# Optimization experiments

Measured on AMD Instinct MI355X. Metric: run time of the kernel, lower is better.

## Reference

```python
import jax, jax.numpy as jnp
import numpy as np

N = 64      # SSM state size (hidden_size)
H = 1024    # channels
L = 2048    # sequence length
BATCH = 8


def setup_inputs() -> dict:
    key = jax.random.key(0)
    ks = jax.random.split(key, 12)
    s = 1.0 / np.sqrt(N)
    n = jnp.arange(N, dtype=jnp.float32)
    return {
        "r": jax.random.normal(ks[0], (BATCH, L, H), dtype=jnp.float32),
        "B_re": jax.random.normal(ks[1], (N,), dtype=jnp.float32) * s,
        "B_im": jax.random.normal(ks[2], (N,), dtype=jnp.float32) * s,
        "C_re": jax.random.normal(ks[3], (H, N), dtype=jnp.float32) * s,
        "C_im": jax.random.normal(ks[4], (H, N), dtype=jnp.float32) * s,
        "P_re": jax.random.normal(ks[5], (N,), dtype=jnp.float32) * s,
        "P_im": jax.random.normal(ks[6], (N,), dtype=jnp.float32) * s,
        "Q_re": jax.random.normal(ks[7], (N,), dtype=jnp.float32) * s,
        "Q_im": jax.random.normal(ks[8], (N,), dtype=jnp.float32) * s,
        # HiPPO-LegS-like diagonal: negative real part for stability, imag ~ pi*n
        "diag_re": -0.5 * jnp.ones((N,), dtype=jnp.float32),
        "diag_im": jnp.pi * (n - N / 2.0),
        "step": jnp.array([1e-3], dtype=jnp.float32),
        "D": jnp.zeros((1,), dtype=jnp.float32),
    }


def _dplr_kernel(Bc, Cc, Pc, Qc, Lam, step, seq_len):
    # Standard S4 DPLR generating function evaluated at roots of unity,
    # then inverse FFT -> real convolution kernel K_c of shape (H, L).
    z = jnp.exp(-2j * jnp.pi * jnp.arange(seq_len) / seq_len).astype(jnp.complex64)  # (L,)
    g = (2.0 / step) * (1.0 - z) / (1.0 + z)                                          # (L,)
    cden = 1.0 / (g[:, None] - Lam[None, :])                                          # (L,N) Cauchy denom
    k00 = jnp.einsum('hn,ln->hl', Cc * Bc, cden)   # (H,L)
    k01 = jnp.einsum('hn,ln->hl', Cc * Pc, cden)   # (H,L)
    k10 = jnp.einsum('n,ln->l', Qc * Bc, cden)     # (L,)
    k11 = jnp.einsum('n,ln->l', Qc * Pc, cden)     # (L,)
    at_roots = (2.0 / (1.0 + z)) * (k00 - k01 * (k10 / (1.0 + k11)))  # (H,L)
    return jnp.fft.ifft(at_roots, axis=-1).real


def reference(r, B_re, B_im, C_re, C_im, P_re, P_im, Q_re, Q_im,
              diag_re, diag_im, step, D):
    step_c = jnp.maximum(step[0], 1e-6)
    Bc = B_re + 1j * B_im
    Cc = C_re + 1j * C_im
    Pc = P_re + 1j * P_im
    Qc = Q_re + 1j * Q_im
    Lam = diag_re + 1j * diag_im
    seq_len = r.shape[1]
    K = _dplr_kernel(Bc, Cc, Pc, Qc, Lam, step_c, seq_len)  # (H, L)
    # causal FFT convolution along the sequence axis
    nfft = 2 * seq_len
    Kf = jnp.fft.rfft(K, n=nfft, axis=-1)            # (H, nfft//2+1)
    uf = jnp.fft.rfft(r, n=nfft, axis=1)             # (B, nfft//2+1, H)
    h1 = jnp.fft.irfft(uf * Kf.T[None], n=nfft, axis=1)[:, :seq_len]  # (B,L,H)
    y1 = h1 + D[0] * r
    return jax.nn.gelu(y1, approximate=False)
```

## Files before the change

kernel.cpp:

```cpp
#include <hip/hip_runtime.h>
#include <math.h>

#define SSM_N 64
#define SSM_H 1024
#define SSM_L 2048
#define SSM_B 8
#define FFTN 2048
#define NT 256
#define KFS 2052

#define PSWZ(a) ((a) ^ (((a) >> 4) & 15))

typedef float f2 __attribute__((ext_vector_type(2)));
static __device__ __forceinline__ f2 mkf2(float a, float b){ f2 v; v.x = a; v.y = b; return v; }

static __device__ __forceinline__ f2 cmul(f2 a, f2 b){
  return mkf2(-a.y, a.y) * mkf2(b.y, b.x) + mkf2(a.x, a.x) * b;
}
static __device__ __forceinline__ f2 cconj(f2 a){ return mkf2(a.x, -a.y); }

template<bool INV> static __device__ __forceinline__ f2 mul_mi(f2 a){
  return INV ? mkf2(-a.y, a.x) : mkf2(a.y, -a.x);
}
template<bool INV> static __device__ __forceinline__ f2 mul_w81(f2 a){
  const float r = 0.70710678118654752440f;
  return INV ? (r * mkf2(a.x - a.y, a.y + a.x)) : (r * mkf2(a.x + a.y, a.y - a.x));
}
template<bool INV> static __device__ __forceinline__ f2 mul_w83(f2 a){
  const float r = 0.70710678118654752440f;
  return INV ? (r * mkf2(-(a.x + a.y), a.x - a.y)) : (r * mkf2(a.y - a.x, -(a.x + a.y)));
}

#define W8C0 1.f
#define W8S0 0.f
#define W8C1 0.92387953251f
#define W8S1 (-0.38268343236f)
#define W8C2 0.70710678119f
#define W8S2 (-0.70710678119f)
#define W8C3 0.38268343236f
#define W8S3 (-0.92387953251f)
#define W8C4 0.f
#define W8S4 (-1.f)
#define W8C5 (-0.38268343236f)
#define W8S5 (-0.92387953251f)
#define W8C6 (-0.70710678119f)
#define W8S6 (-0.70710678119f)
#define W8C7 (-0.92387953251f)
#define W8S7 (-0.38268343236f)

template<bool INV>
static __device__ __forceinline__ void bfly8_store(f2* __restrict__ dst, const f2* __restrict__ tw,
                                                   f2* x, int j, int base, int S)
{
  f2 t0=x[0]+x[4], t4=x[0]-x[4];
  f2 t1=x[1]+x[5], t5=x[1]-x[5];
  f2 t2=x[2]+x[6], t6=x[2]-x[6];
  f2 t3=x[3]+x[7], t7=x[3]-x[7];
  f2 b0=t0+t2, b2=t0-t2, b1=t1+t3, b3=t1-t3;
  f2 mb3 = mul_mi<INV>(b3);
  f2 y0=b0+b1, y4=b0-b1, y2=b2+mb3, y6=b2-mb3;
  f2 v1 = mul_w81<INV>(t5), v2 = mul_mi<INV>(t6), v3 = mul_w83<INV>(t7);
  f2 a0=t4+v2, a2=t4-v2, a1=v1+v3, a3=v1-v3;
  f2 ma3 = mul_mi<INV>(a3);
  f2 y1=a0+a1, y5=a0-a1, y3=a2+ma3, y7=a2-ma3;
  f2 w1 = tw[j];
  if (INV) w1.y = -w1.y;
  f2 w2 = cmul(w1,w1);
  f2 w3 = cmul(w2,w1);
  f2 w4 = cmul(w2,w2);
  f2 w5 = cmul(w3,w2);
  f2 w6 = cmul(w3,w3);
  f2 w7 = cmul(w4,w3);
  dst[PSWZ(base)]     = y0;
  dst[PSWZ(base+S)]   = cmul(y1,w1);
  dst[PSWZ(base+2*S)] = cmul(y2,w2);
  dst[PSWZ(base+3*S)] = cmul(y3,w3);
  dst[PSWZ(base+4*S)] = cmul(y4,w4);
  dst[PSWZ(base+5*S)] = cmul(y5,w5);
  dst[PSWZ(base+6*S)] = cmul(y6,w6);
  dst[PSWZ(base+7*S)] = cmul(y7,w7);
}

template<bool INV, bool ZTOP>
static __device__ __forceinline__ void stage8_first(const f2* __restrict__ src, f2* __restrict__ dst,
                                                    const f2* __restrict__ tw, int t, int st)
{
  const f2* sp = src + st;
  f2 x[8];
  if (ZTOP) {
    #pragma unroll
    for (int q = 0; q < 4; ++q) { x[q] = sp[256*q]; x[q+4] = mkf2(0.f, 0.f); }
  } else {
    #pragma unroll
    for (int q = 0; q < 8; ++q) x[q] = sp[256*q];
  }
  bfly8_store<INV>(dst, tw, x, t, t*8, 1);
}

template<bool INV, int S>
static __device__ __forceinline__ void stage8_mid(const f2* __restrict__ src, f2* __restrict__ dst,
                                                  const f2* __restrict__ tw, int t, int st)
{
  const f2* sp = src + st;
  f2 x[8];
  #pragma unroll
  for (int q = 0; q < 8; ++q) x[q] = sp[256*q];
  int i = t & (S-1);
  int j = t - i;
  bfly8_store<INV>(dst, tw, x, j, i + j*8, S);
}

template<bool INV, bool HALFOUT>
static __device__ __forceinline__ void stage4f(const f2* __restrict__ src, f2* __restrict__ dst, int st)
{
  #pragma unroll
  for (int hh = 0; hh < 2; ++hh) {
    const f2* sp = src + st + 256*hh;
    f2* wp = dst + st + 256*hh;
    f2 x0=sp[0], x1=sp[512], x2=sp[1024], x3=sp[1536];
    f2 a0=x0+x2, a2=x0-x2, a1=x1+x3, a3=x1-x3;
    f2 m = mul_mi<INV>(a3);
    wp[0]   = a0+a1;
    wp[512] = a2+m;
    if (!HALFOUT) {
      wp[1024] = a0-a1;
      wp[1536] = a2-m;
    }
  }
}

template<bool INV, bool ZTOP, bool HALFOUT>
static __device__ void fft2048(f2* A, f2* B, const f2* tw, int t, int st)
{
  __syncthreads();
  stage8_first<INV, ZTOP>(A, B, tw, t, st);
  __syncthreads();
  stage8_mid<INV, 8>(B, A, tw, t, st);
  __syncthreads();
  stage8_mid<INV, 64>(A, B, tw, t, st);
  __syncthreads();
  stage4f<INV, HALFOUT>(B, A, st);
  __syncthreads();
}

static __device__ __forceinline__ void init_tw(f2* tw, int t)
{
  float s, c;
  sincosf(-6.2831853071795864769f * (float)t / (float)FFTN, &s, &c);
  tw[t] = mkf2(c, s);
}

__global__ __launch_bounds__(256) void kernel_cden(
    const float* __restrict__ B_re, const float* __restrict__ B_im,
    const float* __restrict__ P_re, const float* __restrict__ P_im,
    const float* __restrict__ Q_re, const float* __restrict__ Q_im,
    const float* __restrict__ diag_re, const float* __restrict__ diag_im,
    const float* __restrict__ step,
    f2* __restrict__ cdenT, f2* __restrict__ f2v, f2* __restrict__ facv)
{
  int gid = blockIdx.x * blockDim.x + threadIdx.x;
  int l = gid >> 3, s = gid & 7;
  double stepc = (double)step[0]; if (stepc < 1e-6) stepc = 1e-6;
  double ang = -2.0 * 3.14159265358979323846 * (double)l / (double)SSM_L;
  double zr = cos(ang), zi = sin(ang);
  double dr = 1.0 + zr, di = zi;
  double nr = 1.0 - zr, ni = -zi;
  double den = dr*dr + di*di;
  double i2s = 2.0 / stepc;
  double gr = i2s * (nr*dr + ni*di) / den;
  double gi = i2s * (ni*dr - nr*di) / den;
  double k10r=0.0, k10i=0.0, k11r=0.0, k11i=0.0;
  #pragma unroll
  for (int q = 0; q < 8; ++q) {
    int n = s*8 + q;
    double ar = gr - (double)diag_re[n];
    double ai = gi - (double)diag_im[n];
    double d2 = ar*ar + ai*ai;
    double cr = ar/d2, ci = -ai/d2;
    cdenT[n*SSM_L + l] = mkf2((float)cr, (float)ci);
    double qr = (double)Q_re[n], qi = (double)Q_im[n];
    double br = (double)B_re[n], bi = (double)B_im[n];
    double pr = (double)P_re[n], pi = (double)P_im[n];
    double qbr = qr*br - qi*bi, qbi = qr*bi + qi*br;
    double qpr = qr*pr - qi*pi, qpi = qr*pi + qi*pr;
    k10r += qbr*cr - qbi*ci; k10i += qbr*ci + qbi*cr;
    k11r += qpr*cr - qpi*ci; k11i += qpr*ci + qpi*cr;
  }
  #pragma unroll
  for (int off = 1; off < 8; off <<= 1) {
    k10r += __shfl_xor(k10r, off);
    k10i += __shfl_xor(k10i, off);
    k11r += __shfl_xor(k11r, off);
    k11i += __shfl_xor(k11i, off);
  }
  if (s == 0) {
    f2v[l] = mkf2((float)(2.0*dr/den), (float)(-2.0*di/den));
    double er = 1.0 + k11r, ei = k11i;
    double ed = er*er + ei*ei;
    facv[l] = mkf2((float)((k10r*er + k10i*ei)/ed), (float)((k10i*er - k10r*ei)/ed));
  }
}

__global__ __launch_bounds__(NT, 2) void kgemm(
    const float* __restrict__ C_re, const float* __restrict__ C_im,
    const float* __restrict__ B_re, const float* __restrict__ B_im,
    const float* __restrict__ P_re, const float* __restrict__ P_im,
    const f2* __restrict__ cdenT, const f2* __restrict__ f2v, const f2* __restrict__ facv,
    f2* __restrict__ atr)
{
  __shared__ f2 cbs[256];
  int t = threadIdx.x;
  int h0 = blockIdx.x * 2;
  if (t < 128) {
    int h = h0 + (t >> 6), n = t & 63;
    f2 cc = mkf2(C_re[h*SSM_N + n], C_im[h*SSM_N + n]);
    cbs[t]       = cmul(cc, mkf2(B_re[n], B_im[n]));
    cbs[128 + t] = cmul(cc, mkf2(P_re[n], P_im[n]));
  }
  __syncthreads();
  f2 k00[2][8], k01[2][8];
  #pragma unroll
  for (int h = 0; h < 2; ++h)
    #pragma unroll
    for (int i = 0; i < 8; ++i) { k00[h][i] = mkf2(0.f,0.f); k01[h][i] = mkf2(0.f,0.f); }
  for (int n = 0; n < SSM_N; ++n) {
    f2 cd[8];
    #pragma unroll
    for (int i = 0; i < 8; ++i) cd[i] = cdenT[n*SSM_L + t + i*NT];
    #pragma unroll
    for (int h = 0; h < 2; ++h) {
      f2 cb = cbs[h*64 + n], cp = cbs[128 + h*64 + n];
      #pragma unroll
      for (int i = 0; i < 8; ++i) {
        k00[h][i] = k00[h][i] + cmul(cb, cd[i]);
        k01[h][i] = k01[h][i] + cmul(cp, cd[i]);
      }
    }
  }
  #pragma unroll
  for (int h = 0; h < 2; ++h) {
    f2* arow = atr + (size_t)(h0 + h) * SSM_L;
    #pragma unroll
    for (int i = 0; i < 8; ++i) {
      int l = t + i*NT;
      arow[l] = cmul(f2v[l], k00[h][i] - cmul(k01[h][i], facv[l]));
    }
  }
}

__global__ __launch_bounds__(NT, 4) void kfft(const f2* __restrict__ atr, f2* __restrict__ Kf)
{
  __shared__ f2 bufA[FFTN];
  __shared__ f2 bufB[FFTN];
  __shared__ f2 tw[256];
  int t = threadIdx.x;
  int st = PSWZ(t);
  int h = blockIdx.x;
  init_tw(tw, t);
  const f2* arow = atr + (size_t)h * SSM_L;
  #pragma unroll
  for (int i = 0; i < 8; ++i) {
    int n = t + i*NT;
    bufA[PSWZ(n)] = arow[n];
  }
  fft2048<true, false, false>(bufA, bufB, tw, t, st);
  float sb, cb;
  sincosf(-3.14159265358979f * (float)t / (float)FFTN, &sb, &cb);
  f2 base = mkf2(cb, sb);
  const float scale = 1.0f / (float)FFTN;
  {
    const float Wc[8] = {W8C0,W8C1,W8C2,W8C3,W8C4,W8C5,W8C6,W8C7};
    const float Ws[8] = {W8S0,W8S1,W8S2,W8S3,W8S4,W8S5,W8S6,W8S7};
    #pragma unroll
    for (int i = 0; i < 8; ++i) {
      int n = t + i*NT;
      float K = bufA[PSWZ(n)].x * scale;
      f2 c = cmul(base, mkf2(Wc[i], Ws[i]));
      bufB[PSWZ(n)] = K * c;
    }
  }
  fft2048<false, false, true>(bufB, bufA, tw, t, st);
  f2* krow = Kf + (size_t)h * KFS;
  #pragma unroll
  for (int i = 0; i < 4; ++i) {
    int m = t + i*NT;
    krow[2*m+1] = bufB[PSWZ(m)];
  }
  #pragma unroll
  for (int i = 0; i < 4; ++i) {
    int m = t + i*NT;
    if (m == 0) {
      krow[0]    = mkf2(arow[0].x, 0.f);
      krow[FFTN] = mkf2(arow[FFTN/2].x, 0.f);
    } else {
      krow[2*m] = 0.5f * (arow[m] + cconj(arow[FFTN - m]));
    }
  }
}

__global__ __launch_bounds__(256) void ktranspose(const float* __restrict__ src, float* __restrict__ dst)
{
  __shared__ float til[64][65];
  int t = threadIdx.x, tx = t & 15, ty = t >> 4;
  int h0 = blockIdx.x * 64, l0 = blockIdx.y * 64, b = blockIdx.z;
  const float4* s4 = (const float4*)(src + ((size_t)b*SSM_L + l0)*SSM_H + h0);
  #pragma unroll
  for (int i = 0; i < 4; ++i) {
    int lr = ty + 16*i;
    float4 v = s4[(size_t)lr*(SSM_H/4) + tx];
    til[lr][4*tx+0]=v.x; til[lr][4*tx+1]=v.y; til[lr][4*tx+2]=v.z; til[lr][4*tx+3]=v.w;
  }
  __syncthreads();
  float4* d4 = (float4*)(dst + ((size_t)b*SSM_H + h0)*SSM_L + l0);
  #pragma unroll
  for (int i = 0; i < 4; ++i) {
    int hr = ty + 16*i;
    float4 w;
    w.x = til[4*tx+0][hr]; w.y = til[4*tx+1][hr];
    w.z = til[4*tx+2][hr]; w.w = til[4*tx+3][hr];
    d4[(size_t)hr*(SSM_L/4) + tx] = w;
  }
}

__global__ __launch_bounds__(NT, 4) void kernel_conv(float* __restrict__ rT, const f2* __restrict__ Kf,
                                                     const float* __restrict__ Dp)
{
  __shared__ f2 bufA[FFTN];
  __shared__ f2 bufB[FFTN];
  __shared__ f2 tw[256];
  int t = threadIdx.x;
  int st = PSWZ(t);
  int row = blockIdx.x;
  int h = row & (SSM_H - 1);
  float Dv = Dp[0];
  init_tw(tw, t);
  float* rrow = rT + (size_t)row * SSM_L;
  const float4* r4 = (const float4*)rrow;
  float4 vin[2];
  #pragma unroll
  for (int i = 0; i < 2; ++i) {
    int j2 = t + i*NT;
    vin[i] = r4[j2];
    bufA[PSWZ(2*j2)]   = mkf2(vin[i].x, vin[i].y);
    bufA[PSWZ(2*j2+1)] = mkf2(vin[i].z, vin[i].w);
  }
  fft2048<false, true, false>(bufA, bufB, tw, t, st);
  const f2* krow = Kf + (size_t)h * KFS;
  float sb, cb;
  sincosf(-3.14159265358979f * (float)t / (float)FFTN, &sb, &cb);
  f2 base = mkf2(cb, sb);
  {
    const float Wc[4] = {W8C0,W8C1,W8C2,W8C3};
    const float Ws[4] = {W8S0,W8S1,W8S2,W8S3};
    #pragma unroll
    for (int i = 0; i < 4; ++i) {
      int k = t + i*NT;
      f2 w = cmul(base, mkf2(Wc[i], Ws[i]));
      float c = w.x, s = w.y;
      if (k == 0) {
        f2 c0 = bufA[0];
        float F0 = c0.x + c0.y, Fn = c0.x - c0.y;
        f2 K0 = krow[0], Kn = krow[FFTN];
        f2 G0 = F0 * K0;
        f2 Gn = Fn * Kn;
        f2 Xe = 0.5f * (G0 + Gn);
        f2 Xo = 0.5f * (G0 - Gn);
        bufB[0] = mkf2(Xe.x - Xo.y, Xe.y + Xo.x);
        f2 Gm = cmul(cconj(bufA[PSWZ(FFTN/2)]), krow[FFTN/2]);
        bufB[PSWZ(FFTN/2)] = cconj(Gm);
      } else {
        int kk = FFTN - k;
        f2 Ck = bufA[PSWZ(k)], Ckk = bufA[PSWZ(kk)];
        f2 E = mkf2(0.5f*(Ck.x + Ckk.x), 0.5f*(Ck.y - Ckk.y));
        f2 O = mkf2(0.5f*(Ck.y + Ckk.y), 0.5f*(Ckk.x - Ck.x));
        f2 Fk  = E + cmul(mkf2(c, s), O);
        f2 Fkk = cconj(E) + cmul(mkf2(-c, s), cconj(O));
        f2 Gk  = cmul(Fk,  krow[k]);
        f2 Gkk = cmul(Fkk, krow[kk]);
        f2 Xe  = mkf2(0.5f*(Gk.x + Gkk.x), 0.5f*(Gk.y - Gkk.y));
        f2 Dd  = mkf2(0.5f*(Gk.x - Gkk.x), 0.5f*(Gk.y + Gkk.y));
        f2 Xo  = cmul(mkf2(c, -s), Dd);
        bufB[PSWZ(k)] = mkf2(Xe.x - Xo.y, Xe.y + Xo.x);
        f2 Xe2 = mkf2(0.5f*(Gkk.x + Gk.x), 0.5f*(Gkk.y - Gk.y));
        f2 Dd2 = mkf2(0.5f*(Gkk.x - Gk.x), 0.5f*(Gkk.y + Gk.y));
        f2 Xo2 = cmul(mkf2(-c, -s), Dd2);
        bufB[PSWZ(kk)] = mkf2(Xe2.x - Xo2.y, Xe2.y + Xo2.x);
      }
    }
  }
  fft2048<true, false, true>(bufB, bufA, tw, t, st);
  const float sc = 1.0f / (float)FFTN;
  float4* w4 = (float4*)rrow;
  #pragma unroll
  for (int i = 0; i < 2; ++i) {
    int j2 = t + i*NT;
    f2 z0 = bufB[PSWZ(2*j2)], z1 = bufB[PSWZ(2*j2+1)];
    w4[j2] = make_float4(z0.x*sc + Dv*vin[i].x, z0.y*sc + Dv*vin[i].y,
                         z1.x*sc + Dv*vin[i].z, z1.y*sc + Dv*vin[i].w);
  }
}

__global__ __launch_bounds__(256) void ktback(const float* __restrict__ yT, float* __restrict__ out)
{
  __shared__ float til[64][65];
  int t = threadIdx.x, tx = t & 15, ty = t >> 4;
  int h0 = blockIdx.x * 64, l0 = blockIdx.y * 64, b = blockIdx.z;
  const float4* s4 = (const float4*)(yT + ((size_t)b*SSM_H + h0)*SSM_L + l0);
  #pragma unroll
  for (int i = 0; i < 4; ++i) {
    int hr = ty + 16*i;
    float4 v = s4[(size_t)hr*(SSM_L/4) + tx];
    til[hr][4*tx+0]=v.x; til[hr][4*tx+1]=v.y; til[hr][4*tx+2]=v.z; til[hr][4*tx+3]=v.w;
  }
  __syncthreads();
  float4* d4 = (float4*)(out + ((size_t)b*SSM_L + l0)*SSM_H + h0);
  #pragma unroll
  for (int i = 0; i < 4; ++i) {
    int lr = ty + 16*i;
    float4 w;
    float x0 = til[4*tx+0][lr], x1 = til[4*tx+1][lr];
    float x2 = til[4*tx+2][lr], x3 = til[4*tx+3][lr];
    w.x = 0.5f * x0 * (1.0f + erff(x0 * 0.70710678118654752f));
    w.y = 0.5f * x1 * (1.0f + erff(x1 * 0.70710678118654752f));
    w.z = 0.5f * x2 * (1.0f + erff(x2 * 0.70710678118654752f));
    w.w = 0.5f * x3 * (1.0f + erff(x3 * 0.70710678118654752f));
    d4[(size_t)lr*(SSM_H/4) + tx] = w;
  }
}

extern "C" void kernel_launch(void* const* d_in, const int* in_sizes, int n_in,
                              void* d_out, int out_size, void* d_ws, size_t ws_size,
                              hipStream_t stream)
{
  const float* r       = (const float*)d_in[0];
  const float* B_re    = (const float*)d_in[1];
  const float* B_im    = (const float*)d_in[2];
  const float* C_re    = (const float*)d_in[3];
  const float* C_im    = (const float*)d_in[4];
  const float* P_re    = (const float*)d_in[5];
  const float* P_im    = (const float*)d_in[6];
  const float* Q_re    = (const float*)d_in[7];
  const float* Q_im    = (const float*)d_in[8];
  const float* diag_re = (const float*)d_in[9];
  const float* diag_im = (const float*)d_in[10];
  const float* step    = (const float*)d_in[11];
  const float* Dp      = (const float*)d_in[12];
  float* out = (float*)d_out;

  char* p = (char*)d_ws;
  float* rT  = (float*)p; p += (size_t)SSM_B*SSM_H*SSM_L*sizeof(float);
  f2* cdenT  = (f2*)p;    p += (size_t)SSM_N*SSM_L*sizeof(f2);
  f2* f2v    = (f2*)p;    p += (size_t)SSM_L*sizeof(f2);
  f2* facv   = (f2*)p;    p += (size_t)SSM_L*sizeof(f2);
  f2* Kf     = (f2*)p;    p += (size_t)SSM_H*KFS*sizeof(f2);
  f2* atr = (f2*)rT;

  kernel_cden<<<SSM_L*8/NT, NT, 0, stream>>>(B_re, B_im, P_re, P_im, Q_re, Q_im,
                                             diag_re, diag_im, step, cdenT, f2v, facv);
  kgemm<<<SSM_H/2, NT, 0, stream>>>(C_re, C_im, B_re, B_im, P_re, P_im,
                                    cdenT, f2v, facv, atr);
  kfft<<<SSM_H, NT, 0, stream>>>(atr, Kf);
  ktranspose<<<dim3(SSM_H/64, SSM_L/64, SSM_B), 256, 0, stream>>>(r, rT);
  kernel_conv<<<SSM_B*SSM_H, NT, 0, stream>>>(rT, Kf, Dp);
  ktback<<<dim3(SSM_H/64, SSM_L/64, SSM_B), 256, 0, stream>>>(rT, out);
}
```

Baseline: 287.3 us.

## Fuse transpose with Cauchy prep, fuse kernel GEMM with FFT, reorder conv blocks

Merges the input transpose and the Cauchy-denominator computation into one launch, and fuses the DPLR GEMM with the kernel FFT so the intermediate at_roots row stays in shared memory instead of going through global memory. The conv grid is remapped so the 8 batch rows sharing one channel run as adjacent blocks, which improves cache reuse of each Kf row. This removes two launches and a global round-trip. In exchange the kkern block now carries 2x2048 f2 shared buffers plus heavy GEMM register use at launch bound 2, and it processes two FFTs serially per block across only 512 blocks.

```diff
diff --git a/kernel.cpp b/kernel.cpp
--- a/kernel.cpp
+++ b/kernel.cpp
@@ -150,7 +150,8 @@
   tw[t] = mkf2(c, s);
 }
 
-__global__ __launch_bounds__(256) void kernel_cden(
+__global__ __launch_bounds__(256) void kprep(
+    const float* __restrict__ r, float* __restrict__ rT,
     const float* __restrict__ B_re, const float* __restrict__ B_im,
     const float* __restrict__ P_re, const float* __restrict__ P_im,
     const float* __restrict__ Q_re, const float* __restrict__ Q_im,
@@ -158,59 +159,88 @@
     const float* __restrict__ step,
     f2* __restrict__ cdenT, f2* __restrict__ f2v, f2* __restrict__ facv)
 {
-  int gid = blockIdx.x * blockDim.x + threadIdx.x;
-  int l = gid >> 3, s = gid & 7;
-  double stepc = (double)step[0]; if (stepc < 1e-6) stepc = 1e-6;
-  double ang = -2.0 * 3.14159265358979323846 * (double)l / (double)SSM_L;
-  double zr = cos(ang), zi = sin(ang);
-  double dr = 1.0 + zr, di = zi;
-  double nr = 1.0 - zr, ni = -zi;
-  double den = dr*dr + di*di;
-  double i2s = 2.0 / stepc;
-  double gr = i2s * (nr*dr + ni*di) / den;
-  double gi = i2s * (ni*dr - nr*di) / den;
-  double k10r=0.0, k10i=0.0, k11r=0.0, k11i=0.0;
-  #pragma unroll
-  for (int q = 0; q < 8; ++q) {
-    int n = s*8 + q;
-    double ar = gr - (double)diag_re[n];
-    double ai = gi - (double)diag_im[n];
-    double d2 = ar*ar + ai*ai;
-    double cr = ar/d2, ci = -ai/d2;
-    cdenT[n*SSM_L + l] = mkf2((float)cr, (float)ci);
-    double qr = (double)Q_re[n], qi = (double)Q_im[n];
-    double br = (double)B_re[n], bi = (double)B_im[n];
-    double pr = (double)P_re[n], pi = (double)P_im[n];
-    double qbr = qr*br - qi*bi, qbi = qr*bi + qi*br;
-    double qpr = qr*pr - qi*pi, qpi = qr*pi + qi*pr;
-    k10r += qbr*cr - qbi*ci; k10i += qbr*ci + qbi*cr;
-    k11r += qpr*cr - qpi*ci; k11i += qpr*ci + qpi*cr;
-  }
-  #pragma unroll
-  for (int off = 1; off < 8; off <<= 1) {
-    k10r += __shfl_xor(k10r, off);
-    k10i += __shfl_xor(k10i, off);
-    k11r += __shfl_xor(k11r, off);
-    k11i += __shfl_xor(k11i, off);
-  }
-  if (s == 0) {
-    f2v[l] = mkf2((float)(2.0*dr/den), (float)(-2.0*di/den));
-    double er = 1.0 + k11r, ei = k11i;
-    double ed = er*er + ei*ei;
-    facv[l] = mkf2((float)((k10r*er + k10i*ei)/ed), (float)((k10i*er - k10r*ei)/ed));
-  }
-}
-
-__global__ __launch_bounds__(NT, 2) void kgemm(
+  __shared__ float til[64][65];
+  int bid = blockIdx.x;
+  int t = threadIdx.x;
+  if (bid < 4096) {
+    int tx = t & 15, ty = t >> 4;
+    int h0 = (bid & 15) * 64, l0 = ((bid >> 4) & 31) * 64, b = bid >> 9;
+    const float4* s4 = (const float4*)(r + ((size_t)b*SSM_L + l0)*SSM_H + h0);
+    #pragma unroll
+    for (int i = 0; i < 4; ++i) {
+      int lr = ty + 16*i;
+      float4 v = s4[(size_t)lr*(SSM_H/4) + tx];
+      til[lr][4*tx+0]=v.x; til[lr][4*tx+1]=v.y; til[lr][4*tx+2]=v.z; til[lr][4*tx+3]=v.w;
+    }
+    __syncthreads();
+    float4* d4 = (float4*)(rT + ((size_t)b*SSM_H + h0)*SSM_L + l0);
+    #pragma unroll
+    for (int i = 0; i < 4; ++i) {
+      int hr = ty + 16*i;
+      float4 w;
+      w.x = til[4*tx+0][hr]; w.y = til[4*tx+1][hr];
+      w.z = til[4*tx+2][hr]; w.w = til[4*tx+3][hr];
+      d4[(size_t)hr*(SSM_L/4) + tx] = w;
+    }
+  } else {
+    int gid = (bid - 4096) * 256 + t;
+    int l = gid >> 3, s = gid & 7;
+    double stepc = (double)step[0]; if (stepc < 1e-6) stepc = 1e-6;
+    double ang = -2.0 * 3.14159265358979323846 * (double)l / (double)SSM_L;
+    double zr = cos(ang), zi = sin(ang);
+    double dr = 1.0 + zr, di = zi;
+    double nr = 1.0 - zr, ni = -zi;
+    double den = dr*dr + di*di;
+    double i2s = 2.0 / stepc;
+    double gr = i2s * (nr*dr + ni*di) / den;
+    double gi = i2s * (ni*dr - nr*di) / den;
+    double k10r=0.0, k10i=0.0, k11r=0.0, k11i=0.0;
+    #pragma unroll
+    for (int q = 0; q < 8; ++q) {
+      int n = s*8 + q;
+      double ar = gr - (double)diag_re[n];
+      double ai = gi - (double)diag_im[n];
+      double d2 = ar*ar + ai*ai;
+      double cr = ar/d2, ci = -ai/d2;
+      cdenT[n*SSM_L + l] = mkf2((float)cr, (float)ci);
+      double qr = (double)Q_re[n], qi = (double)Q_im[n];
+      double br = (double)B_re[n], bi = (double)B_im[n];
+      double pr = (double)P_re[n], pi = (double)P_im[n];
+      double qbr = qr*br - qi*bi, qbi = qr*bi + qi*br;
+      double qpr = qr*pr - qi*pi, qpi = qr*pi + qi*pr;
+      k10r += qbr*cr - qbi*ci; k10i += qbr*ci + qbi*cr;
+      k11r += qpr*cr - qpi*ci; k11i += qpr*ci + qpi*cr;
+    }
+    #pragma unroll
+    for (int off = 1; off < 8; off <<= 1) {
+      k10r += __shfl_xor(k10r, off);
+      k10i += __shfl_xor(k10i, off);
+      k11r += __shfl_xor(k11r, off);
+      k11i += __shfl_xor(k11i, off);
+    }
+    if (s == 0) {
+      f2v[l] = mkf2((float)(2.0*dr/den), (float)(-2.0*di/den));
+      double er = 1.0 + k11r, ei = k11i;
+      double ed = er*er + ei*ei;
+      facv[l] = mkf2((float)((k10r*er + k10i*ei)/ed), (float)((k10i*er - k10r*ei)/ed));
+    }
+  }
+}
+
+__global__ __launch_bounds__(NT, 2) void kkern(
     const float* __restrict__ C_re, const float* __restrict__ C_im,
     const float* __restrict__ B_re, const float* __restrict__ B_im,
     const float* __restrict__ P_re, const float* __restrict__ P_im,
     const f2* __restrict__ cdenT, const f2* __restrict__ f2v, const f2* __restrict__ facv,
-    f2* __restrict__ atr)
-{
-  __shared__ f2 cbs[256];
-  int t = threadIdx.x;
+    f2* __restrict__ Kf)
+{
+  __shared__ f2 bufA[FFTN];
+  __shared__ f2 bufB[FFTN];
+  __shared__ f2 tw[256];
+  int t = threadIdx.x, st = PSWZ(t);
   int h0 = blockIdx.x * 2;
+  init_tw(tw, t);
+  f2* cbs = bufA;
   if (t < 128) {
     int h = h0 + (t >> 6), n = t & 63;
     f2 cc = mkf2(C_re[h*SSM_N + n], C_im[h*SSM_N + n]);
@@ -237,104 +267,60 @@
       }
     }
   }
-  #pragma unroll
-  for (int h = 0; h < 2; ++h) {
-    f2* arow = atr + (size_t)(h0 + h) * SSM_L;
+  const float Wc8[8] = {W8C0,W8C1,W8C2,W8C3,W8C4,W8C5,W8C6,W8C7};
+  const float Ws8[8] = {W8S0,W8S1,W8S2,W8S3,W8S4,W8S5,W8S6,W8S7};
+  float sb, cb2;
+  sincosf(-3.14159265358979f * (float)t / (float)FFTN, &sb, &cb2);
+  f2 cbase = mkf2(cb2, sb);
+  for (int hh = 0; hh < 2; ++hh) {
+    __syncthreads();
     #pragma unroll
     for (int i = 0; i < 8; ++i) {
       int l = t + i*NT;
-      arow[l] = cmul(f2v[l], k00[h][i] - cmul(k01[h][i], facv[l]));
-    }
-  }
-}
-
-__global__ __launch_bounds__(NT, 4) void kfft(const f2* __restrict__ atr, f2* __restrict__ Kf)
+      f2 fv = f2v[l], fc = facv[l];
+      bufA[PSWZ(l)] = cmul(fv, k00[hh][i] - cmul(k01[hh][i], fc));
+    }
+    __syncthreads();
+    f2* krow = Kf + (size_t)(h0 + hh) * KFS;
+    #pragma unroll
+    for (int i = 0; i < 4; ++i) {
+      int m = t + i*NT;
+      if (m == 0) {
+        krow[0]    = mkf2(bufA[0].x, 0.f);
+        krow[FFTN] = mkf2(bufA[PSWZ(FFTN/2)].x, 0.f);
+      } else {
+        krow[2*m] = 0.5f * (bufA[PSWZ(m)] + cconj(bufA[PSWZ(FFTN - m)]));
+      }
+    }
+    fft2048<true, false, false>(bufA, bufB, tw, t, st);
+    const float scale = 1.0f / (float)FFTN;
+    #pragma unroll
+    for (int i = 0; i < 8; ++i) {
+      int n = t + i*NT;
+      float K = bufA[PSWZ(n)].x * scale;
+      bufA[PSWZ(n)] = K * cmul(cbase, mkf2(Wc8[i], Ws8[i]));
+    }
+    fft2048<false, false, true>(bufA, bufB, tw, t, st);
+    #pragma unroll
+    for (int i = 0; i < 4; ++i) {
+      int m = t + i*NT;
+      krow[2*m+1] = bufA[PSWZ(m)];
+    }
+  }
+}
+
+__global__ __launch_bounds__(NT, 4) void kconv(float* __restrict__ rT, const f2* __restrict__ Kf,
+                                               const float* __restrict__ Dp)
 {
   __shared__ f2 bufA[FFTN];
   __shared__ f2 bufB[FFTN];
   __shared__ f2 tw[256];
-  int t = threadIdx.x;
-  int st = PSWZ(t);
-  int h = blockIdx.x;
-  init_tw(tw, t);
-  const f2* arow = atr + (size_t)h * SSM_L;
-  #pragma unroll
-  for (int i = 0; i < 8; ++i) {
-    int n = t + i*NT;
-    bufA[PSWZ(n)] = arow[n];
-  }
-  fft2048<true, false, false>(bufA, bufB, tw, t, st);
-  float sb, cb;
-  sincosf(-3.14159265358979f * (float)t / (float)FFTN, &sb, &cb);
-  f2 base = mkf2(cb, sb);
-  const float scale = 1.0f / (float)FFTN;
-  {
-    const float Wc[8] = {W8C0,W8C1,W8C2,W8C3,W8C4,W8C5,W8C6,W8C7};
-    const float Ws[8] = {W8S0,W8S1,W8S2,W8S3,W8S4,W8S5,W8S6,W8S7};
-    #pragma unroll
-    for (int i = 0; i < 8; ++i) {
-      int n = t + i*NT;
-      float K = bufA[PSWZ(n)].x * scale;
-      f2 c = cmul(base, mkf2(Wc[i], Ws[i]));
-      bufB[PSWZ(n)] = K * c;
-    }
-  }
-  fft2048<false, false, true>(bufB, bufA, tw, t, st);
-  f2* krow = Kf + (size_t)h * KFS;
-  #pragma unroll
-  for (int i = 0; i < 4; ++i) {
-    int m = t + i*NT;
-    krow[2*m+1] = bufB[PSWZ(m)];
-  }
-  #pragma unroll
-  for (int i = 0; i < 4; ++i) {
-    int m = t + i*NT;
-    if (m == 0) {
-      krow[0]    = mkf2(arow[0].x, 0.f);
-      krow[FFTN] = mkf2(arow[FFTN/2].x, 0.f);
-    } else {
-      krow[2*m] = 0.5f * (arow[m] + cconj(arow[FFTN - m]));
-    }
-  }
-}
-
-__global__ __launch_bounds__(256) void ktranspose(const float* __restrict__ src, float* __restrict__ dst)
-{
-  __shared__ float til[64][65];
-  int t = threadIdx.x, tx = t & 15, ty = t >> 4;
-  int h0 = blockIdx.x * 64, l0 = blockIdx.y * 64, b = blockIdx.z;
-  const float4* s4 = (const float4*)(src + ((size_t)b*SSM_L + l0)*SSM_H + h0);
-  #pragma unroll
-  for (int i = 0; i < 4; ++i) {
-    int lr = ty + 16*i;
-    float4 v = s4[(size_t)lr*(SSM_H/4) + tx];
-    til[lr][4*tx+0]=v.x; til[lr][4*tx+1]=v.y; til[lr][4*tx+2]=v.z; til[lr][4*tx+3]=v.w;
-  }
-  __syncthreads();
-  float4* d4 = (float4*)(dst + ((size_t)b*SSM_H + h0)*SSM_L + l0);
-  #pragma unroll
-  for (int i = 0; i < 4; ++i) {
-    int hr = ty + 16*i;
-    float4 w;
-    w.x = til[4*tx+0][hr]; w.y = til[4*tx+1][hr];
-    w.z = til[4*tx+2][hr]; w.w = til[4*tx+3][hr];
-    d4[(size_t)hr*(SSM_L/4) + tx] = w;
-  }
-}
-
-__global__ __launch_bounds__(NT, 4) void kernel_conv(float* __restrict__ rT, const f2* __restrict__ Kf,
-                                                     const float* __restrict__ Dp)
-{
-  __shared__ f2 bufA[FFTN];
-  __shared__ f2 bufB[FFTN];
-  __shared__ f2 tw[256];
-  int t = threadIdx.x;
-  int st = PSWZ(t);
-  int row = blockIdx.x;
-  int h = row & (SSM_H - 1);
+  int t = threadIdx.x, st = PSWZ(t);
+  int h = blockIdx.x >> 3;
+  int b = blockIdx.x & 7;
   float Dv = Dp[0];
   init_tw(tw, t);
-  float* rrow = rT + (size_t)row * SSM_L;
+  float* rrow = rT + ((size_t)b*SSM_H + h) * SSM_L;
   const float4* r4 = (const float4*)rrow;
   float4 vin[2];
   #pragma unroll
@@ -360,9 +346,8 @@
       if (k == 0) {
         f2 c0 = bufA[0];
         float F0 = c0.x + c0.y, Fn = c0.x - c0.y;
-        f2 K0 = krow[0], Kn = krow[FFTN];
-        f2 G0 = F0 * K0;
-        f2 Gn = Fn * Kn;
+        f2 G0 = F0 * krow[0];
+        f2 Gn = Fn * krow[FFTN];
         f2 Xe = 0.5f * (G0 + Gn);
         f2 Xo = 0.5f * (G0 - Gn);
         bufB[0] = mkf2(Xe.x - Xo.y, Xe.y + Xo.x);
@@ -453,14 +438,11 @@
   f2* f2v    = (f2*)p;    p += (size_t)SSM_L*sizeof(f2);
   f2* facv   = (f2*)p;    p += (size_t)SSM_L*sizeof(f2);
   f2* Kf     = (f2*)p;    p += (size_t)SSM_H*KFS*sizeof(f2);
-  f2* atr = (f2*)rT;
-
-  kernel_cden<<<SSM_L*8/NT, NT, 0, stream>>>(B_re, B_im, P_re, P_im, Q_re, Q_im,
-                                             diag_re, diag_im, step, cdenT, f2v, facv);
-  kgemm<<<SSM_H/2, NT, 0, stream>>>(C_re, C_im, B_re, B_im, P_re, P_im,
-                                    cdenT, f2v, facv, atr);
-  kfft<<<SSM_H, NT, 0, stream>>>(atr, Kf);
-  ktranspose<<<dim3(SSM_H/64, SSM_L/64, SSM_B), 256, 0, stream>>>(r, rT);
-  kernel_conv<<<SSM_B*SSM_H, NT, 0, stream>>>(rT, Kf, Dp);
+
+  kprep<<<4096 + 64, 256, 0, stream>>>(r, rT, B_re, B_im, P_re, P_im, Q_re, Q_im,
+                                       diag_re, diag_im, step, cdenT, f2v, facv);
+  kkern<<<SSM_H/2, NT, 0, stream>>>(C_re, C_im, B_re, B_im, P_re, P_im,
+                                    cdenT, f2v, facv, Kf);
+  kconv<<<SSM_B*SSM_H, NT, 0, stream>>>(rT, Kf, Dp);
   ktback<<<dim3(SSM_H/64, SSM_L/64, SSM_B), 256, 0, stream>>>(rT, out);
 }
```

Measured after the change: 271.3 us. -5.6%, faster.
